# Kernel tuning notes

Hardware: AMD Instinct MI355X
Metric: run time of the kernel (lower is better)

## Reference

```python
import jax, jax.numpy as jnp
import numpy as np

NUM_NODES = 100000
D = 256            # node_hidden_dim
H = 256            # edge_hidden_dim
P = 524288         # num_pairs


def setup_inputs() -> dict:
    key = jax.random.key(0)
    k1, k2, k3, k4, k5, k6 = jax.random.split(key, 6)
    h_nodes = jax.random.normal(k1, (NUM_NODES, D), dtype=jnp.float32)
    dst = jax.random.randint(k2, (P,), 0, NUM_NODES, dtype=jnp.int64)
    src = jax.random.randint(k3, (P,), 0, NUM_NODES, dtype=jnp.int64)
    # Bias-free MLP weights, stored as [in, out] so forward is x @ W
    s1 = 1.0 / np.sqrt(2 * D)
    s2 = 1.0 / np.sqrt(H)
    W1 = jax.random.uniform(k4, (2 * D, H), jnp.float32, -s1, s1)
    W2 = jax.random.uniform(k5, (H, H), jnp.float32, -s2, s2)
    W3 = jax.random.uniform(k6, (H, 2), jnp.float32, -s2, s2)
    return {"h_nodes": h_nodes, "dst": dst, "src": src, "W1": W1, "W2": W2, "W3": W3}


def reference(h_nodes, dst, src, W1, W2, W3):
    # gather src/dst embeddings and concat -> [P, 2D]
    h_pair = jnp.concatenate([h_nodes[dst], h_nodes[src]], axis=-1)
    x = jax.nn.relu(h_pair @ W1)   # [P, H]
    x = jax.nn.relu(x @ W2)        # [P, H]
    return x @ W3                  # [P, 2] edge logits
```

## Files before the change

kernel.cpp:

```cpp
#include <hip/hip_runtime.h>
#include <stdint.h>

typedef __attribute__((ext_vector_type(8))) short short8;
typedef __attribute__((ext_vector_type(4))) float floatx4;

__device__ __forceinline__ unsigned short f2bf(float x) {
  unsigned int u = __float_as_uint(x);
  u += 0x7fffu + ((u >> 16) & 1u);
  return (unsigned short)(u >> 16);
}
__device__ __forceinline__ float bf2f(unsigned short b) {
  return __uint_as_float(((unsigned int)b) << 16);
}

__global__ void hcvt_kernel(const float* __restrict__ h,
                            unsigned short* __restrict__ o, int total8) {
  int u = blockIdx.x * 256 + threadIdx.x;
  if (u >= total8) return;
  const float4* h4 = (const float4*)h;
  float4 v0 = h4[u * 2], v1 = h4[u * 2 + 1];
  short8 s;
  s[0] = (short)f2bf(v0.x); s[1] = (short)f2bf(v0.y);
  s[2] = (short)f2bf(v0.z); s[3] = (short)f2bf(v0.w);
  s[4] = (short)f2bf(v1.x); s[5] = (short)f2bf(v1.y);
  s[6] = (short)f2bf(v1.z); s[7] = (short)f2bf(v1.w);
  ((short8*)o)[u] = s;
}

__global__ void wfrag_kernel(const float* __restrict__ W,
                             unsigned short* __restrict__ out, int total) {
  int u = blockIdx.x * 256 + threadIdx.x;
  if (u >= total) return;
  int j   = u & 7;
  int kq  = (u >> 3) & 3;
  int n   = (u >> 5) & 255;
  int k32 = u >> 13;
  int k   = k32 * 32 + kq * 8 + j;
  out[u] = f2bf(W[k * 256 + n]);
}

template <bool HBF>
__global__ __launch_bounds__(256, 2)
void edge_mlp_kernel(const void* __restrict__ hsrc,
                     const int* __restrict__ dst,
                     const int* __restrict__ src,
                     const unsigned short* __restrict__ W1F,
                     const unsigned short* __restrict__ W2F,
                     const float* __restrict__ W3,
                     float* __restrict__ out) {
  __shared__ unsigned short A[64 * 512];
  __shared__ float w3s[512];
  __shared__ int ioff[128];
  unsigned short* X = A;

  const int t    = threadIdx.x;
  const int lane = t & 63;
  const int w    = t >> 6;
  const int lq   = lane >> 4;
  const int lm   = lane & 15;
  const int m0   = blockIdx.x * 64;

  if (t < 64)       ioff[t] = dst[m0 + t];
  else if (t < 128) ioff[t] = src[m0 + t - 64];
  w3s[t] = W3[t];
  w3s[t + 256] = W3[t + 256];
  __syncthreads();

  {
    const int c    = lane;
    const int half = (c >= 32) ? 64 : 0;
    const int cc   = c & 31;
#pragma unroll
    for (int it = 0; it < 16; ++it) {
      int r = it * 4 + w;
      int node = ioff[half + r];
      short8 v;
      if (HBF) {
        v = ((const short8*)hsrc)[node * 32 + cc];
      } else {
        const float4* h4 = (const float4*)hsrc;
        float4 v0 = h4[node * 64 + cc * 2];
        float4 v1 = h4[node * 64 + cc * 2 + 1];
        v[0] = (short)f2bf(v0.x); v[1] = (short)f2bf(v0.y);
        v[2] = (short)f2bf(v0.z); v[3] = (short)f2bf(v0.w);
        v[4] = (short)f2bf(v1.x); v[5] = (short)f2bf(v1.y);
        v[6] = (short)f2bf(v1.z); v[7] = (short)f2bf(v1.w);
      }
      *(short8*)&A[r * 512 + ((c ^ (r & 7)) << 3)] = v;
    }
  }

  floatx4 acc[4][4];
#pragma unroll
  for (int i = 0; i < 4; ++i)
#pragma unroll
    for (int j = 0; j < 4; ++j) acc[i][j] = (floatx4)(0.0f);

  __syncthreads();

  const short8* B1 = (const short8*)W1F;
  const short8* B2 = (const short8*)W2F;

  auto loadB1 = [&](short8* b, int k32) {
#pragma unroll
    for (int jt = 0; jt < 4; ++jt)
      b[jt] = B1[(k32 * 256 + w * 64 + jt * 16 + lm) * 4 + lq];
  };
  auto stepL1 = [&](int k32, const short8* b) {
    short8 af[4];
#pragma unroll
    for (int i = 0; i < 4; ++i) {
      int r = i * 16 + lm;
      int c = k32 * 4 + lq;
      af[i] = *(const short8*)&A[r * 512 + ((c ^ (r & 7)) << 3)];
    }
#pragma unroll
    for (int i = 0; i < 4; ++i)
#pragma unroll
      for (int j = 0; j < 4; ++j)
        acc[i][j] = __builtin_amdgcn_mfma_f32_16x16x32_bf16(af[i], b[j], acc[i][j], 0, 0, 0);
  };

  {
    short8 b0[4], b1[4];
    loadB1(b0, 0);
#pragma unroll
    for (int k2 = 0; k2 < 8; ++k2) {
      loadB1(b1, k2 * 2 + 1);
      stepL1(k2 * 2, b0);
      loadB1(b0, (k2 * 2 + 2) & 15);
      stepL1(k2 * 2 + 1, b1);
    }
  }

  __syncthreads();
#pragma unroll
  for (int i = 0; i < 4; ++i) {
    int row0 = i * 16 + lq * 4;
#pragma unroll
    for (int j = 0; j < 4; ++j) {
      int col = w * 64 + j * 16 + lm;
      int cch = col >> 3, ce = col & 7;
#pragma unroll
      for (int rg = 0; rg < 4; ++rg) {
        int row = row0 + rg;
        float v = acc[i][j][rg];
        v = v > 0.0f ? v : 0.0f;
        X[row * 256 + (((cch ^ (row & 7)) << 3) | ce)] = f2bf(v);
      }
    }
  }
#pragma unroll
  for (int i = 0; i < 4; ++i)
#pragma unroll
    for (int j = 0; j < 4; ++j) acc[i][j] = (floatx4)(0.0f);
  __syncthreads();

  auto loadB2 = [&](short8* b, int k32) {
#pragma unroll
    for (int jt = 0; jt < 4; ++jt)
      b[jt] = B2[(k32 * 256 + w * 64 + jt * 16 + lm) * 4 + lq];
  };
  auto stepL2 = [&](int k32, const short8* b) {
    short8 af[4];
#pragma unroll
    for (int i = 0; i < 4; ++i) {
      int r = i * 16 + lm;
      int c = k32 * 4 + lq;
      af[i] = *(const short8*)&X[r * 256 + ((c ^ (r & 7)) << 3)];
    }
#pragma unroll
    for (int i = 0; i < 4; ++i)
#pragma unroll
      for (int j = 0; j < 4; ++j)
        acc[i][j] = __builtin_amdgcn_mfma_f32_16x16x32_bf16(af[i], b[j], acc[i][j], 0, 0, 0);
  };

  {
    short8 b0[4], b1[4];
    loadB2(b0, 0);
#pragma unroll
    for (int k2 = 0; k2 < 4; ++k2) {
      loadB2(b1, k2 * 2 + 1);
      stepL2(k2 * 2, b0);
      loadB2(b0, (k2 * 2 + 2) & 7);
      stepL2(k2 * 2 + 1, b1);
    }
  }

  __syncthreads();
#pragma unroll
  for (int i = 0; i < 4; ++i) {
    int row0 = i * 16 + lq * 4;
#pragma unroll
    for (int j = 0; j < 4; ++j) {
      int col = w * 64 + j * 16 + lm;
      int cch = col >> 3, ce = col & 7;
#pragma unroll
      for (int rg = 0; rg < 4; ++rg) {
        int row = row0 + rg;
        float v = acc[i][j][rg];
        v = v > 0.0f ? v : 0.0f;
        X[row * 256 + (((cch ^ (row & 7)) << 3) | ce)] = f2bf(v);
      }
    }
  }
  __syncthreads();

  {
    int r = t >> 2, o = (t >> 1) & 1, hh = t & 1;
    float s = 0.0f;
#pragma unroll
    for (int it = 0; it < 16; ++it) {
      int c = hh * 16 + it;
      short8 xv = *(const short8*)&X[r * 256 + ((c ^ (r & 7)) << 3)];
#pragma unroll
      for (int e = 0; e < 8; ++e)
        s += bf2f((unsigned short)xv[e]) * w3s[((c << 3) + e) * 2 + o];
    }
    s += __shfl_xor(s, 1);
    if (hh == 0) out[(m0 + r) * 2 + o] = s;
  }
}

extern "C" void kernel_launch(void* const* d_in, const int* in_sizes, int n_in,
                              void* d_out, int out_size, void* d_ws, size_t ws_size,
                              hipStream_t stream) {
  const float* h   = (const float*)d_in[0];
  const int*   dst = (const int*)d_in[1];
  const int*   src = (const int*)d_in[2];
  const float* W1  = (const float*)d_in[3];
  const float* W2  = (const float*)d_in[4];
  const float* W3  = (const float*)d_in[5];
  float* out = (float*)d_out;

  const int h_elems  = in_sizes[0];
  const int n_pairs  = in_sizes[1];
  const int grid     = n_pairs / 64;

  const size_t hbf_elems = (size_t)h_elems;
  const bool use_hbf = ws_size >= (hbf_elems + 131072 + 65536) * sizeof(unsigned short);

  unsigned short* HBF = (unsigned short*)d_ws;
  unsigned short* W1F = use_hbf ? HBF + hbf_elems : (unsigned short*)d_ws;
  unsigned short* W2F = W1F + 131072;

  wfrag_kernel<<<512, 256, 0, stream>>>(W1, W1F, 131072);
  wfrag_kernel<<<256, 256, 0, stream>>>(W2, W2F, 65536);

  if (use_hbf) {
    int total8 = h_elems / 8;
    hcvt_kernel<<<(total8 + 255) / 256, 256, 0, stream>>>(h, HBF, total8);
    edge_mlp_kernel<true><<<grid, 256, 0, stream>>>(HBF, dst, src, W1F, W2F, W3, out);
  } else {
    edge_mlp_kernel<false><<<grid, 256, 0, stream>>>(h, dst, src, W1F, W2F, W3, out);
  }
}
```

Measured before the change: 464.5 us.

## Make edge MLP kernel persistent with register-prefetched next-tile gather

Converts the edge MLP kernel into a persistent grid-stride kernel capped at 512 blocks, each processing many 64-pair tiles. The gather of the next tile's node rows is issued into registers (16 short8 per thread) before the current tile's two MFMA layers run, and indices are double-buffered two tiles ahead. This aims to hide gather latency behind compute. In exchange it adds 64 VGPRs of live prefetch state, which may raise register pressure against the launch bound of 2 blocks per CU, and the fixed grid may not match the CU count.

New measurement: 1.187 ms. 2.56x slower.

```diff
diff --git a/kernel.cpp b/kernel.cpp
--- a/kernel.cpp
+++ b/kernel.cpp
@@ -47,10 +47,10 @@
                      const unsigned short* __restrict__ W1F,
                      const unsigned short* __restrict__ W2F,
                      const float* __restrict__ W3,
-                     float* __restrict__ out) {
+                     float* __restrict__ out, int ntiles) {
   __shared__ unsigned short A[64 * 512];
   __shared__ float w3s[512];
-  __shared__ int ioff[128];
+  __shared__ int iobuf[2][128];
   unsigned short* X = A;
 
   const int t    = threadIdx.x;
@@ -58,168 +58,194 @@
   const int w    = t >> 6;
   const int lq   = lane >> 4;
   const int lm   = lane & 15;
-  const int m0   = blockIdx.x * 64;
-
-  if (t < 64)       ioff[t] = dst[m0 + t];
-  else if (t < 128) ioff[t] = src[m0 + t - 64];
+  const int bid  = blockIdx.x;
+  const int stride = gridDim.x;
+  const int nIter  = (ntiles - bid + stride - 1) / stride;
+
   w3s[t] = W3[t];
   w3s[t + 256] = W3[t + 256];
-  __syncthreads();
-
-  {
-    const int c    = lane;
-    const int half = (c >= 32) ? 64 : 0;
-    const int cc   = c & 31;
+  if (t < 128) {
+    const int* p = (t < 64) ? dst : src;
+    iobuf[0][t] = p[bid * 64 + (t & 63)];
+    if (nIter > 1) iobuf[1][t] = p[(bid + stride) * 64 + (t & 63)];
+  }
+
+  const short8* B1 = (const short8*)W1F;
+  const short8* B2 = (const short8*)W2F;
+
+  short8 g[16];
+  auto issue_gather = [&](int nb) {
+    const int half = (lane >= 32) ? 64 : 0;
+    const int cc   = lane & 31;
 #pragma unroll
     for (int it = 0; it < 16; ++it) {
       int r = it * 4 + w;
-      int node = ioff[half + r];
-      short8 v;
+      int node = iobuf[nb][half + r];
       if (HBF) {
-        v = ((const short8*)hsrc)[node * 32 + cc];
+        g[it] = ((const short8*)hsrc)[node * 32 + cc];
       } else {
         const float4* h4 = (const float4*)hsrc;
         float4 v0 = h4[node * 64 + cc * 2];
         float4 v1 = h4[node * 64 + cc * 2 + 1];
-        v[0] = (short)f2bf(v0.x); v[1] = (short)f2bf(v0.y);
-        v[2] = (short)f2bf(v0.z); v[3] = (short)f2bf(v0.w);
-        v[4] = (short)f2bf(v1.x); v[5] = (short)f2bf(v1.y);
-        v[6] = (short)f2bf(v1.z); v[7] = (short)f2bf(v1.w);
-      }
-      *(short8*)&A[r * 512 + ((c ^ (r & 7)) << 3)] = v;
-    }
-  }
-
-  floatx4 acc[4][4];
-#pragma unroll
-  for (int i = 0; i < 4; ++i)
-#pragma unroll
-    for (int j = 0; j < 4; ++j) acc[i][j] = (floatx4)(0.0f);
+        short8 s;
+        s[0] = (short)f2bf(v0.x); s[1] = (short)f2bf(v0.y);
+        s[2] = (short)f2bf(v0.z); s[3] = (short)f2bf(v0.w);
+        s[4] = (short)f2bf(v1.x); s[5] = (short)f2bf(v1.y);
+        s[6] = (short)f2bf(v1.z); s[7] = (short)f2bf(v1.w);
+        g[it] = s;
+      }
+    }
+  };
 
   __syncthreads();
-
-  const short8* B1 = (const short8*)W1F;
-  const short8* B2 = (const short8*)W2F;
-
-  auto loadB1 = [&](short8* b, int k32) {
-#pragma unroll
-    for (int jt = 0; jt < 4; ++jt)
-      b[jt] = B1[(k32 * 256 + w * 64 + jt * 16 + lm) * 4 + lq];
-  };
-  auto stepL1 = [&](int k32, const short8* b) {
-    short8 af[4];
-#pragma unroll
-    for (int i = 0; i < 4; ++i) {
-      int r = i * 16 + lm;
-      int c = k32 * 4 + lq;
-      af[i] = *(const short8*)&A[r * 512 + ((c ^ (r & 7)) << 3)];
-    }
-#pragma unroll
-    for (int i = 0; i < 4; ++i)
-#pragma unroll
-      for (int j = 0; j < 4; ++j)
-        acc[i][j] = __builtin_amdgcn_mfma_f32_16x16x32_bf16(af[i], b[j], acc[i][j], 0, 0, 0);
-  };
-
-  {
-    short8 b0[4], b1[4];
-    loadB1(b0, 0);
-#pragma unroll
-    for (int k2 = 0; k2 < 8; ++k2) {
-      loadB1(b1, k2 * 2 + 1);
-      stepL1(k2 * 2, b0);
-      loadB1(b0, (k2 * 2 + 2) & 15);
-      stepL1(k2 * 2 + 1, b1);
-    }
-  }
-
-  __syncthreads();
-#pragma unroll
-  for (int i = 0; i < 4; ++i) {
-    int row0 = i * 16 + lq * 4;
-#pragma unroll
-    for (int j = 0; j < 4; ++j) {
-      int col = w * 64 + j * 16 + lm;
-      int cch = col >> 3, ce = col & 7;
-#pragma unroll
-      for (int rg = 0; rg < 4; ++rg) {
-        int row = row0 + rg;
-        float v = acc[i][j][rg];
-        v = v > 0.0f ? v : 0.0f;
-        X[row * 256 + (((cch ^ (row & 7)) << 3) | ce)] = f2bf(v);
-      }
-    }
-  }
-#pragma unroll
-  for (int i = 0; i < 4; ++i)
-#pragma unroll
-    for (int j = 0; j < 4; ++j) acc[i][j] = (floatx4)(0.0f);
-  __syncthreads();
-
-  auto loadB2 = [&](short8* b, int k32) {
-#pragma unroll
-    for (int jt = 0; jt < 4; ++jt)
-      b[jt] = B2[(k32 * 256 + w * 64 + jt * 16 + lm) * 4 + lq];
-  };
-  auto stepL2 = [&](int k32, const short8* b) {
-    short8 af[4];
-#pragma unroll
-    for (int i = 0; i < 4; ++i) {
-      int r = i * 16 + lm;
-      int c = k32 * 4 + lq;
-      af[i] = *(const short8*)&X[r * 256 + ((c ^ (r & 7)) << 3)];
-    }
-#pragma unroll
-    for (int i = 0; i < 4; ++i)
-#pragma unroll
-      for (int j = 0; j < 4; ++j)
-        acc[i][j] = __builtin_amdgcn_mfma_f32_16x16x32_bf16(af[i], b[j], acc[i][j], 0, 0, 0);
-  };
-
-  {
-    short8 b0[4], b1[4];
-    loadB2(b0, 0);
-#pragma unroll
-    for (int k2 = 0; k2 < 4; ++k2) {
-      loadB2(b1, k2 * 2 + 1);
-      stepL2(k2 * 2, b0);
-      loadB2(b0, (k2 * 2 + 2) & 7);
-      stepL2(k2 * 2 + 1, b1);
-    }
-  }
-
-  __syncthreads();
-#pragma unroll
-  for (int i = 0; i < 4; ++i) {
-    int row0 = i * 16 + lq * 4;
-#pragma unroll
-    for (int j = 0; j < 4; ++j) {
-      int col = w * 64 + j * 16 + lm;
-      int cch = col >> 3, ce = col & 7;
-#pragma unroll
-      for (int rg = 0; rg < 4; ++rg) {
-        int row = row0 + rg;
-        float v = acc[i][j][rg];
-        v = v > 0.0f ? v : 0.0f;
-        X[row * 256 + (((cch ^ (row & 7)) << 3) | ce)] = f2bf(v);
-      }
-    }
-  }
-  __syncthreads();
-
-  {
-    int r = t >> 2, o = (t >> 1) & 1, hh = t & 1;
-    float s = 0.0f;
-#pragma unroll
-    for (int it = 0; it < 16; ++it) {
-      int c = hh * 16 + it;
-      short8 xv = *(const short8*)&X[r * 256 + ((c ^ (r & 7)) << 3)];
-#pragma unroll
-      for (int e = 0; e < 8; ++e)
-        s += bf2f((unsigned short)xv[e]) * w3s[((c << 3) + e) * 2 + o];
-    }
-    s += __shfl_xor(s, 1);
-    if (hh == 0) out[(m0 + r) * 2 + o] = s;
+  issue_gather(0);
+
+  for (int i = 0; i < nIter; ++i) {
+    const int tile = bid + i * stride;
+    const int m0   = tile * 64;
+    __syncthreads();
+    {
+      const int c = lane;
+#pragma unroll
+      for (int it = 0; it < 16; ++it) {
+        int r = it * 4 + w;
+        *(short8*)&A[r * 512 + ((c ^ (r & 7)) << 3)] = g[it];
+      }
+    }
+    int ioreg = 0;
+    const bool have2 = (i + 2) < nIter;
+    if (have2 && t < 128) {
+      const int* p = (t < 64) ? dst : src;
+      ioreg = p[(bid + (i + 2) * stride) * 64 + (t & 63)];
+    }
+    __syncthreads();
+    if ((i + 1) < nIter) issue_gather((i + 1) & 1);
+    if (have2 && t < 128) iobuf[i & 1][t] = ioreg;
+
+    floatx4 acc[4][4];
+#pragma unroll
+    for (int ii = 0; ii < 4; ++ii)
+#pragma unroll
+      for (int jj = 0; jj < 4; ++jj) acc[ii][jj] = (floatx4)(0.0f);
+
+    auto loadB1 = [&](short8* b, int k32) {
+#pragma unroll
+      for (int jt = 0; jt < 4; ++jt)
+        b[jt] = B1[(k32 * 256 + w * 64 + jt * 16 + lm) * 4 + lq];
+    };
+    auto stepL1 = [&](int k32, const short8* b) {
+      short8 af[4];
+#pragma unroll
+      for (int ii = 0; ii < 4; ++ii) {
+        int r = ii * 16 + lm;
+        int c = k32 * 4 + lq;
+        af[ii] = *(const short8*)&A[r * 512 + ((c ^ (r & 7)) << 3)];
+      }
+#pragma unroll
+      for (int ii = 0; ii < 4; ++ii)
+#pragma unroll
+        for (int jj = 0; jj < 4; ++jj)
+          acc[ii][jj] = __builtin_amdgcn_mfma_f32_16x16x32_bf16(af[ii], b[jj], acc[ii][jj], 0, 0, 0);
+    };
+    {
+      short8 b0[4], b1[4];
+      loadB1(b0, 0);
+#pragma unroll
+      for (int k2 = 0; k2 < 8; ++k2) {
+        loadB1(b1, k2 * 2 + 1);
+        stepL1(k2 * 2, b0);
+        loadB1(b0, (k2 * 2 + 2) & 15);
+        stepL1(k2 * 2 + 1, b1);
+      }
+    }
+
+    __syncthreads();
+#pragma unroll
+    for (int ii = 0; ii < 4; ++ii) {
+      int row0 = ii * 16 + lq * 4;
+#pragma unroll
+      for (int jj = 0; jj < 4; ++jj) {
+        int col = w * 64 + jj * 16 + lm;
+        int cch = col >> 3, ce = col & 7;
+#pragma unroll
+        for (int rg = 0; rg < 4; ++rg) {
+          int row = row0 + rg;
+          float v = acc[ii][jj][rg];
+          v = v > 0.0f ? v : 0.0f;
+          X[row * 256 + (((cch ^ (row & 7)) << 3) | ce)] = f2bf(v);
+        }
+      }
+    }
+#pragma unroll
+    for (int ii = 0; ii < 4; ++ii)
+#pragma unroll
+      for (int jj = 0; jj < 4; ++jj) acc[ii][jj] = (floatx4)(0.0f);
+    __syncthreads();
+
+    auto loadB2 = [&](short8* b, int k32) {
+#pragma unroll
+      for (int jt = 0; jt < 4; ++jt)
+        b[jt] = B2[(k32 * 256 + w * 64 + jt * 16 + lm) * 4 + lq];
+    };
+    auto stepL2 = [&](int k32, const short8* b) {
+      short8 af[4];
+#pragma unroll
+      for (int ii = 0; ii < 4; ++ii) {
+        int r = ii * 16 + lm;
+        int c = k32 * 4 + lq;
+        af[ii] = *(const short8*)&X[r * 256 + ((c ^ (r & 7)) << 3)];
+      }
+#pragma unroll
+      for (int ii = 0; ii < 4; ++ii)
+#pragma unroll
+        for (int jj = 0; jj < 4; ++jj)
+          acc[ii][jj] = __builtin_amdgcn_mfma_f32_16x16x32_bf16(af[ii], b[jj], acc[ii][jj], 0, 0, 0);
+    };
+    {
+      short8 b0[4], b1[4];
+      loadB2(b0, 0);
+#pragma unroll
+      for (int k2 = 0; k2 < 4; ++k2) {
+        loadB2(b1, k2 * 2 + 1);
+        stepL2(k2 * 2, b0);
+        loadB2(b0, (k2 * 2 + 2) & 7);
+        stepL2(k2 * 2 + 1, b1);
+      }
+    }
+
+    __syncthreads();
+#pragma unroll
+    for (int ii = 0; ii < 4; ++ii) {
+      int row0 = ii * 16 + lq * 4;
+#pragma unroll
+      for (int jj = 0; jj < 4; ++jj) {
+        int col = w * 64 + jj * 16 + lm;
+        int cch = col >> 3, ce = col & 7;
+#pragma unroll
+        for (int rg = 0; rg < 4; ++rg) {
+          int row = row0 + rg;
+          float v = acc[ii][jj][rg];
+          v = v > 0.0f ? v : 0.0f;
+          X[row * 256 + (((cch ^ (row & 7)) << 3) | ce)] = f2bf(v);
+        }
+      }
+    }
+    __syncthreads();
+
+    {
+      int r = t >> 2, o = (t >> 1) & 1, hh = t & 1;
+      float s = 0.0f;
+#pragma unroll
+      for (int it = 0; it < 16; ++it) {
+        int c = hh * 16 + it;
+        short8 xv = *(const short8*)&X[r * 256 + ((c ^ (r & 7)) << 3)];
+#pragma unroll
+        for (int e = 0; e < 8; ++e)
+          s += bf2f((unsigned short)xv[e]) * w3s[((c << 3) + e) * 2 + o];
+      }
+      s += __shfl_xor(s, 1);
+      if (hh == 0) out[(m0 + r) * 2 + o] = s;
+    }
   }
 }
 
@@ -234,9 +260,10 @@
   const float* W3  = (const float*)d_in[5];
   float* out = (float*)d_out;
 
-  const int h_elems  = in_sizes[0];
-  const int n_pairs  = in_sizes[1];
-  const int grid     = n_pairs / 64;
+  const int h_elems = in_sizes[0];
+  const int n_pairs = in_sizes[1];
+  const int ntiles  = n_pairs / 64;
+  const int grid    = ntiles < 512 ? ntiles : 512;
 
   const size_t hbf_elems = (size_t)h_elems;
   const bool use_hbf = ws_size >= (hbf_elems + 131072 + 65536) * sizeof(unsigned short);
@@ -251,8 +278,8 @@
   if (use_hbf) {
     int total8 = h_elems / 8;
     hcvt_kernel<<<(total8 + 255) / 256, 256, 0, stream>>>(h, HBF, total8);
-    edge_mlp_kernel<true><<<grid, 256, 0, stream>>>(HBF, dst, src, W1F, W2F, W3, out);
+    edge_mlp_kernel<true><<<grid, 256, 0, stream>>>(HBF, dst, src, W1F, W2F, W3, out, ntiles);
   } else {
-    edge_mlp_kernel<false><<<grid, 256, 0, stream>>>(h, dst, src, W1F, W2F, W3, out);
+    edge_mlp_kernel<false><<<grid, 256, 0, stream>>>(h, dst, src, W1F, W2F, W3, out, ntiles);
   }
 }
```

## Persistent double-buffered edge MLP kernel with async global-to-LDS gather

Applied to the files above, without the earlier changes.

Replaces the one-block-per-tile bf16 path with a persistent kernel of 512 threads over a capped grid of 256 blocks. Each block loops over tiles and double-buffers the gathered node rows in LDS, using global_load_lds to prefetch the next tile's rows while MFMA runs on the current one, and it prefetches indices several tiles ahead. The intent is to hide gather latency behind compute. In exchange, LDS doubles to about 130 KB per block, which likely caps residency at one block per CU, and each wave now computes a narrower 32-column slice.

Result: slower. 930.2 us (+100.2%).

```diff
diff --git a/kernel.cpp b/kernel.cpp
--- a/kernel.cpp
+++ b/kernel.cpp
@@ -11,6 +11,11 @@
 }
 __device__ __forceinline__ float bf2f(unsigned short b) {
   return __uint_as_float(((unsigned int)b) << 16);
+}
+__device__ __forceinline__ void gload_lds16(const void* g, void* lds) {
+  __builtin_amdgcn_global_load_lds(
+      (const __attribute__((address_space(1))) unsigned int*)g,
+      (__attribute__((address_space(3))) unsigned int*)lds, 16, 0, 0);
 }
 
 __global__ void hcvt_kernel(const float* __restrict__ h,
@@ -39,79 +44,239 @@
   out[u] = f2bf(W[k * 256 + n]);
 }
 
-template <bool HBF>
-__global__ __launch_bounds__(256, 2)
-void edge_mlp_kernel(const void* __restrict__ hsrc,
-                     const int* __restrict__ dst,
-                     const int* __restrict__ src,
-                     const unsigned short* __restrict__ W1F,
-                     const unsigned short* __restrict__ W2F,
-                     const float* __restrict__ W3,
-                     float* __restrict__ out) {
-  __shared__ unsigned short A[64 * 512];
+__global__ __launch_bounds__(512, 2)
+void edge_mlp_pipe(const unsigned short* __restrict__ hbf,
+                   const int* __restrict__ dst,
+                   const int* __restrict__ src,
+                   const unsigned short* __restrict__ W1F,
+                   const unsigned short* __restrict__ W2F,
+                   const float* __restrict__ W3,
+                   float* __restrict__ out, int ntiles) {
+  __shared__ unsigned short Abuf[2][64 * 512];
   __shared__ float w3s[512];
-  __shared__ int ioff[128];
-  unsigned short* X = A;
 
   const int t    = threadIdx.x;
   const int lane = t & 63;
   const int w    = t >> 6;
   const int lq   = lane >> 4;
   const int lm   = lane & 15;
-  const int m0   = blockIdx.x * 64;
-
-  if (t < 64)       ioff[t] = dst[m0 + t];
+  const int bid  = blockIdx.x;
+  const int stride = gridDim.x;
+  const int nIter  = (ntiles - bid + stride - 1) / stride;
+  const int last   = nIter - 1;
+
+  w3s[t] = W3[t];
+
+  const int* idxsrc = (w < 4) ? dst : src;
+  int n1[4], n2[4];
+  auto loadIdx = [&](int* n, int it) {
+    int mm = (bid + it * stride) * 64;
+#pragma unroll
+    for (int ii = 0; ii < 4; ++ii) n[ii] = idxsrc[mm + ii * 16 + lm];
+  };
+  auto gatherTo = [&](char* Anx, const int* n, int u) {
+    int frag = w * 8 + u, k32 = frag >> 2, ii = frag & 3;
+    const char* g = (const char*)hbf + (size_t)n[ii] * 512 + (k32 & 7) * 64 + lq * 16;
+    gload_lds16(g, Anx + frag * 1024);
+  };
+
+  {
+    int n0[4];
+    loadIdx(n0, 0);
+    loadIdx(n1, last >= 1 ? 1 : 0);
+    loadIdx(n2, last >= 2 ? 2 : last);
+#pragma unroll
+    for (int u = 0; u < 8; ++u) gatherTo((char*)&Abuf[0][0], n0, u);
+  }
+  __syncthreads();
+
+  const short8* B1 = (const short8*)W1F;
+  const short8* B2 = (const short8*)W2F;
+
+  for (int i = 0; i < nIter; ++i) {
+    const int cur = i & 1;
+    const unsigned short* Ac = &Abuf[cur][0];
+    char* An = (char*)&Abuf[cur ^ 1][0];
+    unsigned short* X = &Abuf[cur][16384];
+    const int m0 = (bid + i * stride) * 64;
+    const bool pre = (i + 1) < nIter;
+
+    floatx4 acc[4][2];
+#pragma unroll
+    for (int ii = 0; ii < 4; ++ii)
+#pragma unroll
+      for (int j = 0; j < 2; ++j) acc[ii][j] = (floatx4)(0.0f);
+
+    short8 bq[4][2];
+#pragma unroll
+    for (int s = 0; s < 4; ++s)
+#pragma unroll
+      for (int j = 0; j < 2; ++j)
+        bq[s][j] = B1[(s * 256 + w * 32 + j * 16 + lm) * 4 + lq];
+
+#pragma unroll
+    for (int s = 0; s < 16; ++s) {
+      if ((s & 1) == 0 && pre) gatherTo(An, n1, s >> 1);
+      short8 af[4];
+#pragma unroll
+      for (int ii = 0; ii < 4; ++ii)
+        af[ii] = ((const short8*)Ac)[(s * 4 + ii) * 64 + lane];
+#pragma unroll
+      for (int ii = 0; ii < 4; ++ii)
+#pragma unroll
+        for (int j = 0; j < 2; ++j)
+          acc[ii][j] = __builtin_amdgcn_mfma_f32_16x16x32_bf16(af[ii], bq[s & 3][j], acc[ii][j], 0, 0, 0);
+      if (s < 12)
+#pragma unroll
+        for (int j = 0; j < 2; ++j)
+          bq[s & 3][j] = B1[((s + 4) * 256 + w * 32 + j * 16 + lm) * 4 + lq];
+    }
+    __syncthreads();
+
+#pragma unroll
+    for (int ii = 0; ii < 4; ++ii) {
+      int row0 = ii * 16 + lq * 4;
+#pragma unroll
+      for (int j = 0; j < 2; ++j) {
+        int col = w * 32 + j * 16 + lm;
+        int c8 = col >> 3, ce = col & 7;
+#pragma unroll
+        for (int rg = 0; rg < 4; ++rg) {
+          int row = row0 + rg;
+          float v = acc[ii][j][rg];
+          v = v > 0.0f ? v : 0.0f;
+          X[row * 256 + (((c8 ^ (row & 7)) << 3) | ce)] = f2bf(v);
+        }
+      }
+    }
+#pragma unroll
+    for (int ii = 0; ii < 4; ++ii) n1[ii] = n2[ii];
+    loadIdx(n2, (i + 3) <= last ? (i + 3) : last);
+
+#pragma unroll
+    for (int ii = 0; ii < 4; ++ii)
+#pragma unroll
+      for (int j = 0; j < 2; ++j) acc[ii][j] = (floatx4)(0.0f);
+    __syncthreads();
+
+    short8 bb[2][2];
+#pragma unroll
+    for (int s = 0; s < 2; ++s)
+#pragma unroll
+      for (int j = 0; j < 2; ++j)
+        bb[s][j] = B2[(s * 256 + w * 32 + j * 16 + lm) * 4 + lq];
+#pragma unroll
+    for (int s = 0; s < 8; ++s) {
+      short8 af[4];
+#pragma unroll
+      for (int ii = 0; ii < 4; ++ii) {
+        int r = ii * 16 + lm, c8 = s * 4 + lq;
+        af[ii] = *(const short8*)&X[r * 256 + ((c8 ^ (r & 7)) << 3)];
+      }
+#pragma unroll
+      for (int ii = 0; ii < 4; ++ii)
+#pragma unroll
+        for (int j = 0; j < 2; ++j)
+          acc[ii][j] = __builtin_amdgcn_mfma_f32_16x16x32_bf16(af[ii], bb[s & 1][j], acc[ii][j], 0, 0, 0);
+      if (s < 6)
+#pragma unroll
+        for (int j = 0; j < 2; ++j)
+          bb[s & 1][j] = B2[((s + 2) * 256 + w * 32 + j * 16 + lm) * 4 + lq];
+    }
+    __syncthreads();
+
+#pragma unroll
+    for (int ii = 0; ii < 4; ++ii) {
+      int row0 = ii * 16 + lq * 4;
+#pragma unroll
+      for (int j = 0; j < 2; ++j) {
+        int col = w * 32 + j * 16 + lm;
+        int c8 = col >> 3, ce = col & 7;
+#pragma unroll
+        for (int rg = 0; rg < 4; ++rg) {
+          int row = row0 + rg;
+          float v = acc[ii][j][rg];
+          v = v > 0.0f ? v : 0.0f;
+          X[row * 256 + (((c8 ^ (row & 7)) << 3) | ce)] = f2bf(v);
+        }
+      }
+    }
+    __syncthreads();
+
+    {
+      int r = t >> 3, o = (t >> 2) & 1, q = t & 3;
+      float s = 0.0f;
+#pragma unroll
+      for (int cc = 0; cc < 8; ++cc) {
+        int c = q * 8 + cc;
+        short8 xv = *(const short8*)&X[r * 256 + ((c ^ (r & 7)) << 3)];
+#pragma unroll
+        for (int e = 0; e < 8; ++e)
+          s += bf2f((unsigned short)xv[e]) * w3s[((c << 3) + e) * 2 + o];
+      }
+      s += __shfl_xor(s, 1);
+      s += __shfl_xor(s, 2);
+      if (q == 0) out[(m0 + r) * 2 + o] = s;
+    }
+    __syncthreads();
+  }
+}
+
+__global__ __launch_bounds__(256, 2)
+void edge_mlp_fb(const float* __restrict__ h,
+                 const int* __restrict__ dst,
+                 const int* __restrict__ src,
+                 const unsigned short* __restrict__ W1F,
+                 const unsigned short* __restrict__ W2F,
+                 const float* __restrict__ W3,
+                 float* __restrict__ out) {
+  __shared__ unsigned short A[64 * 512];
+  __shared__ float w3s[512];
+  __shared__ int ioff[128];
+  unsigned short* X = A;
+
+  const int t = threadIdx.x, lane = t & 63, w = t >> 6;
+  const int lq = lane >> 4, lm = lane & 15;
+  const int m0 = blockIdx.x * 64;
+
+  if (t < 64) ioff[t] = dst[m0 + t];
   else if (t < 128) ioff[t] = src[m0 + t - 64];
   w3s[t] = W3[t];
   w3s[t + 256] = W3[t + 256];
   __syncthreads();
-
   {
-    const int c    = lane;
-    const int half = (c >= 32) ? 64 : 0;
-    const int cc   = c & 31;
+    const int c = lane, half = (c >= 32) ? 64 : 0, cc = c & 31;
 #pragma unroll
     for (int it = 0; it < 16; ++it) {
       int r = it * 4 + w;
       int node = ioff[half + r];
+      const float4* h4 = (const float4*)h;
+      float4 v0 = h4[node * 64 + cc * 2], v1 = h4[node * 64 + cc * 2 + 1];
       short8 v;
-      if (HBF) {
-        v = ((const short8*)hsrc)[node * 32 + cc];
-      } else {
-        const float4* h4 = (const float4*)hsrc;
-        float4 v0 = h4[node * 64 + cc * 2];
-        float4 v1 = h4[node * 64 + cc * 2 + 1];
-        v[0] = (short)f2bf(v0.x); v[1] = (short)f2bf(v0.y);
-        v[2] = (short)f2bf(v0.z); v[3] = (short)f2bf(v0.w);
-        v[4] = (short)f2bf(v1.x); v[5] = (short)f2bf(v1.y);
-        v[6] = (short)f2bf(v1.z); v[7] = (short)f2bf(v1.w);
-      }
+      v[0] = (short)f2bf(v0.x); v[1] = (short)f2bf(v0.y);
+      v[2] = (short)f2bf(v0.z); v[3] = (short)f2bf(v0.w);
+      v[4] = (short)f2bf(v1.x); v[5] = (short)f2bf(v1.y);
+      v[6] = (short)f2bf(v1.z); v[7] = (short)f2bf(v1.w);
       *(short8*)&A[r * 512 + ((c ^ (r & 7)) << 3)] = v;
     }
   }
-
   floatx4 acc[4][4];
 #pragma unroll
   for (int i = 0; i < 4; ++i)
 #pragma unroll
     for (int j = 0; j < 4; ++j) acc[i][j] = (floatx4)(0.0f);
-
-  __syncthreads();
-
+  __syncthreads();
   const short8* B1 = (const short8*)W1F;
   const short8* B2 = (const short8*)W2F;
-
-  auto loadB1 = [&](short8* b, int k32) {
+#pragma unroll
+  for (int k32 = 0; k32 < 16; ++k32) {
+    short8 b[4], af[4];
 #pragma unroll
     for (int jt = 0; jt < 4; ++jt)
       b[jt] = B1[(k32 * 256 + w * 64 + jt * 16 + lm) * 4 + lq];
-  };
-  auto stepL1 = [&](int k32, const short8* b) {
-    short8 af[4];
 #pragma unroll
     for (int i = 0; i < 4; ++i) {
-      int r = i * 16 + lm;
-      int c = k32 * 4 + lq;
+      int r = i * 16 + lm, c = k32 * 4 + lq;
       af[i] = *(const short8*)&A[r * 512 + ((c ^ (r & 7)) << 3)];
     }
 #pragma unroll
@@ -119,34 +284,20 @@
 #pragma unroll
       for (int j = 0; j < 4; ++j)
         acc[i][j] = __builtin_amdgcn_mfma_f32_16x16x32_bf16(af[i], b[j], acc[i][j], 0, 0, 0);
-  };
-
-  {
-    short8 b0[4], b1[4];
-    loadB1(b0, 0);
-#pragma unroll
-    for (int k2 = 0; k2 < 8; ++k2) {
-      loadB1(b1, k2 * 2 + 1);
-      stepL1(k2 * 2, b0);
-      loadB1(b0, (k2 * 2 + 2) & 15);
-      stepL1(k2 * 2 + 1, b1);
-    }
-  }
-
+  }
   __syncthreads();
 #pragma unroll
   for (int i = 0; i < 4; ++i) {
     int row0 = i * 16 + lq * 4;
 #pragma unroll
     for (int j = 0; j < 4; ++j) {
-      int col = w * 64 + j * 16 + lm;
-      int cch = col >> 3, ce = col & 7;
+      int col = w * 64 + j * 16 + lm, c8 = col >> 3, ce = col & 7;
 #pragma unroll
       for (int rg = 0; rg < 4; ++rg) {
         int row = row0 + rg;
         float v = acc[i][j][rg];
         v = v > 0.0f ? v : 0.0f;
-        X[row * 256 + (((cch ^ (row & 7)) << 3) | ce)] = f2bf(v);
+        X[row * 256 + (((c8 ^ (row & 7)) << 3) | ce)] = f2bf(v);
       }
     }
   }
@@ -155,18 +306,15 @@
 #pragma unroll
     for (int j = 0; j < 4; ++j) acc[i][j] = (floatx4)(0.0f);
   __syncthreads();
-
-  auto loadB2 = [&](short8* b, int k32) {
+#pragma unroll
+  for (int k32 = 0; k32 < 8; ++k32) {
+    short8 b[4], af[4];
 #pragma unroll
     for (int jt = 0; jt < 4; ++jt)
       b[jt] = B2[(k32 * 256 + w * 64 + jt * 16 + lm) * 4 + lq];
-  };
-  auto stepL2 = [&](int k32, const short8* b) {
-    short8 af[4];
 #pragma unroll
     for (int i = 0; i < 4; ++i) {
-      int r = i * 16 + lm;
-      int c = k32 * 4 + lq;
+      int r = i * 16 + lm, c = k32 * 4 + lq;
       af[i] = *(const short8*)&X[r * 256 + ((c ^ (r & 7)) << 3)];
     }
 #pragma unroll
@@ -174,39 +322,24 @@
 #pragma unroll
       for (int j = 0; j < 4; ++j)
         acc[i][j] = __builtin_amdgcn_mfma_f32_16x16x32_bf16(af[i], b[j], acc[i][j], 0, 0, 0);
-  };
-
-  {
-    short8 b0[4], b1[4];
-    loadB2(b0, 0);
-#pragma unroll
-    for (int k2 = 0; k2 < 4; ++k2) {
-      loadB2(b1, k2 * 2 + 1);
-      stepL2(k2 * 2, b0);
-      loadB2(b0, (k2 * 2 + 2) & 7);
-      stepL2(k2 * 2 + 1, b1);
-    }
-  }
-
+  }
   __syncthreads();
 #pragma unroll
   for (int i = 0; i < 4; ++i) {
     int row0 = i * 16 + lq * 4;
 #pragma unroll
     for (int j = 0; j < 4; ++j) {
-      int col = w * 64 + j * 16 + lm;
-      int cch = col >> 3, ce = col & 7;
+      int col = w * 64 + j * 16 + lm, c8 = col >> 3, ce = col & 7;
 #pragma unroll
       for (int rg = 0; rg < 4; ++rg) {
         int row = row0 + rg;
         float v = acc[i][j][rg];
         v = v > 0.0f ? v : 0.0f;
-        X[row * 256 + (((cch ^ (row & 7)) << 3) | ce)] = f2bf(v);
-      }
-    }
-  }
-  __syncthreads();
-
+        X[row * 256 + (((c8 ^ (row & 7)) << 3) | ce)] = f2bf(v);
+      }
+    }
+  }
+  __syncthreads();
   {
     int r = t >> 2, o = (t >> 1) & 1, hh = t & 1;
     float s = 0.0f;
@@ -234,9 +367,9 @@
   const float* W3  = (const float*)d_in[5];
   float* out = (float*)d_out;
 
-  const int h_elems  = in_sizes[0];
-  const int n_pairs  = in_sizes[1];
-  const int grid     = n_pairs / 64;
+  const int h_elems = in_sizes[0];
+  const int n_pairs = in_sizes[1];
+  const int ntiles  = n_pairs / 64;
 
   const size_t hbf_elems = (size_t)h_elems;
   const bool use_hbf = ws_size >= (hbf_elems + 131072 + 65536) * sizeof(unsigned short);
@@ -251,8 +384,9 @@
   if (use_hbf) {
     int total8 = h_elems / 8;
     hcvt_kernel<<<(total8 + 255) / 256, 256, 0, stream>>>(h, HBF, total8);
-    edge_mlp_kernel<true><<<grid, 256, 0, stream>>>(HBF, dst, src, W1F, W2F, W3, out);
+    int grid = ntiles < 256 ? ntiles : 256;
+    edge_mlp_pipe<<<grid, 512, 0, stream>>>(HBF, dst, src, W1F, W2F, W3, out, ntiles);
   } else {
-    edge_mlp_kernel<false><<<grid, 256, 0, stream>>>(h, dst, src, W1F, W2F, W3, out);
-  }
-}
+    edge_mlp_fb<<<ntiles, 256, 0, stream>>>(h, dst, src, W1F, W2F, W3, out);
+  }
+}
```
